# Kernel tuning notes

Hardware: AMD Instinct MI355X
Metric: run time of the kernel (lower is better)

Reference implementation:

```python
import jax, jax.numpy as jnp
import numpy as np


def setup_inputs() -> dict:
    key = jax.random.key(0)
    k1, k2 = jax.random.split(key)
    B, C, H, W = 4, 256, 64, 64
    f_m = jax.random.normal(k1, (B, C, H, W), dtype=jnp.float32)
    f_d = jax.random.normal(k2, (B, C, H, W), dtype=jnp.float32)
    return {"f_m": f_m, "f_d": f_d}


def reference(f_m, f_d):
    B, C, H, W = f_d.shape
    HW = H * W
    f_fuse = f_m + f_d                      # [B, C, H, W]
    f_c = f_fuse.reshape(B, C, HW)          # [B, C, HW]
    # scores[b, n, m] = sum_c f_c[b, c, n] * f_c[b, c, m]
    scores = jnp.einsum('bcn,bcm->bnm', f_c, f_c)   # [B, HW, HW]
    att = jax.nn.softmax(scores, axis=-1)           # softmax over last dim
    f_d_r = f_d.reshape(B, C, HW)                   # [B, C, HW]
    # out[b, c, m] = sum_n f_d_r[b, c, n] * att[b, n, m]
    f_d_att = jnp.einsum('bcn,bnm->bcm', f_d_r, att).reshape(B, C, H, W)
    return f_d_att + f_d
```

## Files before the change

### kernel.cpp

```cpp
#include <hip/hip_runtime.h>
#include <math.h>

#define B_ 4
#define C_ 256
#define N_ 4096
#define LDE 68
#define LDX 72

typedef __attribute__((ext_vector_type(8))) short short8;
typedef __attribute__((ext_vector_type(4))) float f32x4;
typedef __attribute__((ext_vector_type(2))) float f32x2;

__device__ inline ushort f2bf(float f) {
    uint u = __float_as_uint(f);
    return (ushort)((u + 0x7fffu + ((u >> 16) & 1u)) >> 16);
}
__device__ inline float bf2f(ushort h) { return __uint_as_float(((uint)h) << 16); }

__device__ inline f32x4 mfma16(short8 a, short8 b, f32x4 c) {
    return __builtin_amdgcn_mfma_f32_16x16x32_bf16(a, b, c, 0, 0, 0);
}
__device__ inline f32x4 mfma8(long a, long b, f32x4 c) {
    return __builtin_amdgcn_mfma_f32_16x16x32_fp8_fp8(a, b, c, 0, 0, 0);
}

__device__ inline size_t xfi8(int b, int nt, int kk) {
    return (((size_t)(b * 256 + nt)) * 8 + kk) * 512;
}
__device__ inline size_t ffi(int b, int nc, int ct, int k2) {
    return ((((size_t)(b * 64 + nc)) * 16 + ct) * 2 + k2) * 512;
}
__device__ inline size_t eti(int b, int mt, int ng) {
    return (((size_t)(b * 256 + mt)) * 512 + (size_t)ng) * 128;
}
__device__ inline size_t zmi(int b, int nc, int mt) {
    return ((size_t)(b * 64 + nc)) * 256 + mt;
}

__global__ __launch_bounds__(256) void prep_x_kernel(const float* __restrict__ fm,
                                                     const float* __restrict__ fd,
                                                     uchar* __restrict__ xfrag8) {
    __shared__ ushort xl[64][LDX];
    const int b = blockIdx.z, c0 = blockIdx.y * 64, n0 = blockIdx.x * 64;
    const int t = threadIdx.x;
    const int n4 = (t & 15) * 4, cl = t >> 4;
    const size_t base = (size_t)b * C_ * N_;
    #pragma unroll
    for (int p = 0; p < 4; ++p) {
        const int cr = 16 * p + cl;
        const float4 m4 = *(const float4*)(fm + base + (size_t)(c0 + cr) * N_ + n0 + n4);
        const float4 d4 = *(const float4*)(fd + base + (size_t)(c0 + cr) * N_ + n0 + n4);
        ushort4 xo;
        xo.x = f2bf(m4.x + d4.x); xo.y = f2bf(m4.y + d4.y);
        xo.z = f2bf(m4.z + d4.z); xo.w = f2bf(m4.w + d4.w);
        *(ushort4*)(&xl[cr][n4]) = xo;
    }
    __syncthreads();
    const int l = t & 63, tl = t >> 6;
    const int nl = 16 * tl + (l & 15);
    #pragma unroll
    for (int j = 0; j < 2; ++j) {
        const int kk = (c0 >> 5) + j;
        const int cb = 32 * j + 8 * (l >> 4);
        float f[8];
        #pragma unroll
        for (int i = 0; i < 8; ++i) f[i] = bf2f(xl[cb + i][nl]);
        int d0 = __builtin_amdgcn_cvt_pk_fp8_f32(f[0], f[1], 0, 0);
        d0 = __builtin_amdgcn_cvt_pk_fp8_f32(f[2], f[3], d0, 1);
        int d1 = __builtin_amdgcn_cvt_pk_fp8_f32(f[4], f[5], 0, 0);
        d1 = __builtin_amdgcn_cvt_pk_fp8_f32(f[6], f[7], d1, 1);
        uint* dst = (uint*)(xfrag8 + xfi8(b, (n0 >> 4) + tl, kk) + (size_t)l * 8);
        dst[0] = (uint)d0; dst[1] = (uint)d1;
    }
}

__global__ __launch_bounds__(512, 2) void lsum_e_kernel(const uchar* __restrict__ xfrag8,
                                                        uchar* __restrict__ E8,
                                                        uchar* __restrict__ zmask,
                                                        float* __restrict__ sinv) {
    __shared__ float red[8][64];
    const int bid = blockIdx.x;
    const int b = (bid >> 1) & 3;
    const int n0 = ((((bid >> 3) << 1) | (bid & 1))) * 64;
    const int t = threadIdx.x, lane = t & 63, w = t >> 6;
    const int l15 = lane & 15, q = lane >> 4;
    const int ph = (bid >> 3) & 31;

    long af[4][8];
    #pragma unroll
    for (int ns = 0; ns < 4; ++ns)
        #pragma unroll
        for (int kk = 0; kk < 8; ++kk)
            af[ns][kk] = *(const long*)(xfrag8 + xfi8(b, (n0 >> 4) + ns, kk) + (size_t)lane * 8);

    float dv[4][4];
    #pragma unroll
    for (int ns = 0; ns < 4; ++ns) {
        f32x4 dacc = {0.f, 0.f, 0.f, 0.f};
        #pragma unroll
        for (int kk = 0; kk < 8; ++kk)
            dacc = mfma8(af[ns][kk], af[ns][kk], dacc);
        #pragma unroll
        for (int r = 0; r < 4; ++r)
            dv[ns][r] = __shfl(dacc[r], 20 * q + r, 64);
    }

    long bn[8];
    #pragma unroll
    for (int kk = 0; kk < 8; ++kk)
        bn[kk] = *(const long*)(xfrag8 + xfi8(b, (ph & 31) * 8 + w, kk) + (size_t)lane * 8);

    const size_t ebl = (size_t)l15 * 8 + 4 * (q & 1);
    const int ngb = (n0 >> 3) + (q >> 1);
    const int ncb = n0 >> 6;

    float rs[4][4] = {};
    for (int mc = 0; mc < 32; ++mc) {
        const int cur = ((mc + ph) & 31) * 8 + w;
        const int nxt = ((mc + 1 + ph) & 31) * 8 + w;
        f32x4 a0 = {0.f,0.f,0.f,0.f}, a1 = {0.f,0.f,0.f,0.f};
        f32x4 a2 = {0.f,0.f,0.f,0.f}, a3 = {0.f,0.f,0.f,0.f};
        __builtin_amdgcn_s_setprio(1);
        #pragma unroll
        for (int kk = 0; kk < 8; ++kk) {
            const long bc = bn[kk];
            a0 = mfma8(af[0][kk], bc, a0);
            a1 = mfma8(af[1][kk], bc, a1);
            a2 = mfma8(af[2][kk], bc, a2);
            a3 = mfma8(af[3][kk], bc, a3);
            bn[kk] = *(const long*)(xfrag8 + xfi8(b, nxt, kk) + (size_t)lane * 8);
        }
        __builtin_amdgcn_s_setprio(0);
        float df[4][4];
#define EDF(AA, NS)                                                    \
        df[NS][0] = AA[0] - dv[NS][0]; df[NS][1] = AA[1] - dv[NS][1];  \
        df[NS][2] = AA[2] - dv[NS][2]; df[NS][3] = AA[3] - dv[NS][3];
        EDF(a0, 0) EDF(a1, 1) EDF(a2, 2) EDF(a3, 3)
#undef EDF
        const float mx = fmaxf(
            fmaxf(fmaxf(fmaxf(df[0][0], df[0][1]), fmaxf(df[0][2], df[0][3])),
                  fmaxf(fmaxf(df[1][0], df[1][1]), fmaxf(df[1][2], df[1][3]))),
            fmaxf(fmaxf(fmaxf(df[2][0], df[2][1]), fmaxf(df[2][2], df[2][3])),
                  fmaxf(fmaxf(df[3][0], df[3][1]), fmaxf(df[3][2], df[3][3]))));
        const bool nz = (__ballot(mx > -30.0f) != 0ULL);
        if (lane == 0) zmask[zmi(b, ncb, cur)] = nz ? 1 : 0;
        if (nz) {
            uint dpk[4];
#define EEXP(NS)                                                                       \
            {                                                                          \
                float e0 = __expf(df[NS][0]), e1 = __expf(df[NS][1]);                  \
                float e2 = __expf(df[NS][2]), e3 = __expf(df[NS][3]);                  \
                rs[NS][0] += e0; rs[NS][1] += e1; rs[NS][2] += e2; rs[NS][3] += e3;    \
                int d = __builtin_amdgcn_cvt_pk_fp8_f32(e0, e1, 0, 0);                 \
                d = __builtin_amdgcn_cvt_pk_fp8_f32(e2, e3, d, 1);                     \
                dpk[NS] = (uint)d;                                                     \
            }
            EEXP(0) EEXP(1) EEXP(2) EEXP(3)
#undef EEXP
            #pragma unroll
            for (int ns = 0; ns < 4; ++ns)
                *(uint*)(E8 + eti(b, cur, ngb + 2 * ns) + ebl) = dpk[ns];
        }
    }
    #pragma unroll
    for (int off = 1; off < 16; off <<= 1)
        #pragma unroll
        for (int ns = 0; ns < 4; ++ns)
            #pragma unroll
            for (int r = 0; r < 4; ++r)
                rs[ns][r] += __shfl_xor(rs[ns][r], off, 64);
    if (l15 == 0) {
        #pragma unroll
        for (int ns = 0; ns < 4; ++ns)
            #pragma unroll
            for (int r = 0; r < 4; ++r)
                red[w][16 * ns + 4 * q + r] = rs[ns][r];
    }
    __syncthreads();
    if (t < 64) {
        float s = 0.f;
        #pragma unroll
        for (int ww = 0; ww < 8; ++ww) s += red[ww][t];
        sinv[b * N_ + n0 + t] = 1.0f / s;
    }
}

__global__ __launch_bounds__(512, 2) void out_e_kernel(const uchar* __restrict__ E8,
                                                       const uchar* __restrict__ zmask,
                                                       const float* __restrict__ sinv,
                                                       const float* __restrict__ fd32,
                                                       float* __restrict__ outp) {
    const int bid = blockIdx.x;
    const int b = (bid >> 1) & 3;
    const int m0 = ((((bid >> 3) << 1) | (bid & 1))) * 64;
    const int t = threadIdx.x, lane = t & 63, w = t >> 6;
    const int l15 = lane & 15, q = lane >> 4;
    const size_t fb = (size_t)b * C_ * N_;
    const uchar* mrow = zmask + zmi(b, 0, m0 >> 4);

    f32x4 acc[2][4];
    #pragma unroll
    for (int ct = 0; ct < 2; ++ct)
        #pragma unroll
        for (int mt = 0; mt < 4; ++mt)
            acc[ct][mt] = (f32x4){0.f, 0.f, 0.f, 0.f};

    for (int g = 0; g < 8; ++g) {
        uint mk[8];
        #pragma unroll
        for (int i = 0; i < 8; ++i)
            mk[i] = *(const uint*)(mrow + (size_t)(8 * g + i) * 256);
        #pragma unroll
        for (int i = 0; i < 8; ++i) {
            if (mk[i] == 0) continue;
            const int nc = 8 * g + i;
            const float* sv = sinv + b * N_ + 64 * nc + 8 * q;
            float4 s0[2], s1[2];
            #pragma unroll
            for (int k2 = 0; k2 < 2; ++k2) {
                s0[k2] = *(const float4*)(sv + 32 * k2);
                s1[k2] = *(const float4*)(sv + 32 * k2 + 4);
            }
            short8 fn[2][2];
            #pragma unroll
            for (int ct = 0; ct < 2; ++ct) {
                const int c = 32 * w + 16 * ct + l15;
                const float* frow = fd32 + fb + (size_t)c * N_ + 64 * nc + 8 * q;
                #pragma unroll
                for (int k2 = 0; k2 < 2; ++k2) {
                    const float4 fa = *(const float4*)(frow + 32 * k2);
                    const float4 fb4 = *(const float4*)(frow + 32 * k2 + 4);
                    union { ushort us[8]; short8 v; } u;
                    u.us[0] = f2bf(fa.x * s0[k2].x); u.us[1] = f2bf(fa.y * s0[k2].y);
                    u.us[2] = f2bf(fa.z * s0[k2].z); u.us[3] = f2bf(fa.w * s0[k2].w);
                    u.us[4] = f2bf(fb4.x * s1[k2].x); u.us[5] = f2bf(fb4.y * s1[k2].y);
                    u.us[6] = f2bf(fb4.z * s1[k2].z); u.us[7] = f2bf(fb4.w * s1[k2].w);
                    fn[ct][k2] = u.v;
                }
            }
            #pragma unroll
            for (int k2 = 0; k2 < 2; ++k2) {
                #pragma unroll
                for (int mt = 0; mt < 4; ++mt) {
                    const long e8 = *(const long*)(E8 + eti(b, (m0 >> 4) + mt, 8 * nc + 4 * k2 + q) + (size_t)l15 * 8);
                    const uint lo = (uint)(unsigned long)e8;
                    const uint hi = (uint)((unsigned long)e8 >> 32);
                    const f32x2 f01 = __builtin_amdgcn_cvt_pk_f32_fp8((int)lo, false);
                    const f32x2 f23 = __builtin_amdgcn_cvt_pk_f32_fp8((int)lo, true);
                    const f32x2 f45 = __builtin_amdgcn_cvt_pk_f32_fp8((int)hi, false);
                    const f32x2 f67 = __builtin_amdgcn_cvt_pk_f32_fp8((int)hi, true);
                    union { uint u[4]; short8 v; } be;
                    asm("v_cvt_pk_bf16_f32 %0, %1, %2" : "=v"(be.u[0]) : "v"(f01.x), "v"(f01.y));
                    asm("v_cvt_pk_bf16_f32 %0, %1, %2" : "=v"(be.u[1]) : "v"(f23.x), "v"(f23.y));
                    asm("v_cvt_pk_bf16_f32 %0, %1, %2" : "=v"(be.u[2]) : "v"(f45.x), "v"(f45.y));
                    asm("v_cvt_pk_bf16_f32 %0, %1, %2" : "=v"(be.u[3]) : "v"(f67.x), "v"(f67.y));
                    acc[0][mt] = mfma16(fn[0][k2], be.v, acc[0][mt]);
                    acc[1][mt] = mfma16(fn[1][k2], be.v, acc[1][mt]);
                }
            }
        }
    }
    #pragma unroll
    for (int ct = 0; ct < 2; ++ct)
        #pragma unroll
        for (int mt = 0; mt < 4; ++mt)
            #pragma unroll
            for (int r = 0; r < 4; ++r) {
                const int c = 32 * w + 16 * ct + 4 * q + r;
                const int m = m0 + 16 * mt + l15;
                const size_t o = fb + (size_t)c * N_ + m;
                outp[o] = acc[ct][mt][r] + fd32[o];
            }
}

__global__ __launch_bounds__(256) void prep_kernel(const float* __restrict__ fm,
                                                   const float* __restrict__ fd,
                                                   uchar* __restrict__ xfrag8,
                                                   ushort* __restrict__ ffrag) {
    __shared__ ushort xl[64][LDX];
    __shared__ ushort fl[64][LDX];
    const int b = blockIdx.z, c0 = blockIdx.y * 64, n0 = blockIdx.x * 64;
    const int t = threadIdx.x;
    const int n4 = (t & 15) * 4, cl = t >> 4;
    const size_t base = (size_t)b * C_ * N_;
    #pragma unroll
    for (int p = 0; p < 4; ++p) {
        const int cr = 16 * p + cl;
        const float4 m4 = *(const float4*)(fm + base + (size_t)(c0 + cr) * N_ + n0 + n4);
        const float4 d4 = *(const float4*)(fd + base + (size_t)(c0 + cr) * N_ + n0 + n4);
        ushort4 fo;
        fo.x = f2bf(d4.x); fo.y = f2bf(d4.y); fo.z = f2bf(d4.z); fo.w = f2bf(d4.w);
        *(ushort4*)(&fl[cr][n4]) = fo;
        ushort4 xo;
        xo.x = f2bf(m4.x + d4.x); xo.y = f2bf(m4.y + d4.y);
        xo.z = f2bf(m4.z + d4.z); xo.w = f2bf(m4.w + d4.w);
        *(ushort4*)(&xl[cr][n4]) = xo;
    }
    __syncthreads();
    const int l = t & 63, tl = t >> 6;
    {
        const int nl = 16 * tl + (l & 15);
        #pragma unroll
        for (int j = 0; j < 2; ++j) {
            const int kk = (c0 >> 5) + j;
            const int cb = 32 * j + 8 * (l >> 4);
            float f[8];
            #pragma unroll
            for (int i = 0; i < 8; ++i) f[i] = bf2f(xl[cb + i][nl]);
            int d0 = __builtin_amdgcn_cvt_pk_fp8_f32(f[0], f[1], 0, 0);
            d0 = __builtin_amdgcn_cvt_pk_fp8_f32(f[2], f[3], d0, 1);
            int d1 = __builtin_amdgcn_cvt_pk_fp8_f32(f[4], f[5], 0, 0);
            d1 = __builtin_amdgcn_cvt_pk_fp8_f32(f[6], f[7], d1, 1);
            uint* dst = (uint*)(xfrag8 + xfi8(b, (n0 >> 4) + tl, kk) + (size_t)l * 8);
            dst[0] = (uint)d0; dst[1] = (uint)d1;
        }
    }
    {
        const int row = 16 * tl + (l & 15);
        #pragma unroll
        for (int k2 = 0; k2 < 2; ++k2) {
            const int col = 32 * k2 + 8 * (l >> 4);
            const ushort4 a0 = *(const ushort4*)(&fl[row][col]);
            const ushort4 a1 = *(const ushort4*)(&fl[row][col + 4]);
            ushort* dst = ffrag + ffi(b, n0 >> 6, (c0 >> 4) + tl, k2) + l * 8;
            *(ushort4*)(dst) = a0; *(ushort4*)(dst + 4) = a1;
        }
    }
}

__global__ __launch_bounds__(512, 2) void lsum_g_kernel(const uchar* __restrict__ xfrag8,
                                                        float* __restrict__ lg) {
    __shared__ float red[8][64];
    __shared__ float dgl[64];
    const int bid = blockIdx.x;
    const int b = (bid >> 1) & 3;
    const int n0 = ((((bid >> 3) << 1) | (bid & 1))) * 64;
    const int t = threadIdx.x, lane = t & 63, w = t >> 6;
    const int l15 = lane & 15, q = lane >> 4;

    long af[4][8];
    #pragma unroll
    for (int ns = 0; ns < 4; ++ns)
        #pragma unroll
        for (int kk = 0; kk < 8; ++kk)
            af[ns][kk] = *(const long*)(xfrag8 + xfi8(b, (n0 >> 4) + ns, kk) + (size_t)lane * 8);

    float dv[4][4];
    #pragma unroll
    for (int ns = 0; ns < 4; ++ns) {
        f32x4 dacc = {0.f, 0.f, 0.f, 0.f};
        #pragma unroll
        for (int kk = 0; kk < 8; ++kk)
            dacc = mfma8(af[ns][kk], af[ns][kk], dacc);
        #pragma unroll
        for (int r = 0; r < 4; ++r)
            dv[ns][r] = __shfl(dacc[r], 20 * q + r, 64);
    }
    if (w == 0 && l15 == 0) {
        #pragma unroll
        for (int ns = 0; ns < 4; ++ns)
            #pragma unroll
            for (int r = 0; r < 4; ++r)
                dgl[16 * ns + 4 * q + r] = dv[ns][r];
    }

    long bn[8];
    #pragma unroll
    for (int kk = 0; kk < 8; ++kk)
        bn[kk] = *(const long*)(xfrag8 + xfi8(b, w, kk) + (size_t)lane * 8);

    float rs[4][4] = {};
    for (int mc = 0; mc < 32; ++mc) {
        const int mtn = (mc + 1 < 32) ? (mc + 1) * 8 + w : w;
        f32x4 a0 = {0.f,0.f,0.f,0.f}, a1 = {0.f,0.f,0.f,0.f};
        f32x4 a2 = {0.f,0.f,0.f,0.f}, a3 = {0.f,0.f,0.f,0.f};
        #pragma unroll
        for (int kk = 0; kk < 8; ++kk) {
            const long bc = bn[kk];
            a0 = mfma8(af[0][kk], bc, a0);
            a1 = mfma8(af[1][kk], bc, a1);
            a2 = mfma8(af[2][kk], bc, a2);
            a3 = mfma8(af[3][kk], bc, a3);
            bn[kk] = *(const long*)(xfrag8 + xfi8(b, mtn, kk) + (size_t)lane * 8);
        }
        #pragma unroll
        for (int r = 0; r < 4; ++r) {
            rs[0][r] += __expf(a0[r] - dv[0][r]);
            rs[1][r] += __expf(a1[r] - dv[1][r]);
            rs[2][r] += __expf(a2[r] - dv[2][r]);
            rs[3][r] += __expf(a3[r] - dv[3][r]);
        }
    }
    #pragma unroll
    for (int off = 1; off < 16; off <<= 1)
        #pragma unroll
        for (int ns = 0; ns < 4; ++ns)
            #pragma unroll
            for (int r = 0; r < 4; ++r)
                rs[ns][r] += __shfl_xor(rs[ns][r], off, 64);
    if (l15 == 0) {
        #pragma unroll
        for (int ns = 0; ns < 4; ++ns)
            #pragma unroll
            for (int r = 0; r < 4; ++r)
                red[w][16 * ns + 4 * q + r] = rs[ns][r];
    }
    __syncthreads();
    if (t < 64) {
        float s = 0.f;
        #pragma unroll
        for (int ww = 0; ww < 8; ++ww) s += red[ww][t];
        lg[b * N_ + n0 + t] = dgl[t] + __logf(s);
    }
}

__global__ __launch_bounds__(512, 2) void out_g_kernel(const uchar* __restrict__ xfrag8,
                                                       const ushort* __restrict__ ffrag,
                                                       const float* __restrict__ gg,
                                                       const float* __restrict__ fd32,
                                                       float* __restrict__ outp) {
    __shared__ ushort ET[2][64][LDE];
    const int bid = blockIdx.x;
    const int b = (bid >> 1) & 3;
    const int m0 = ((((bid >> 3) << 1) | (bid & 1))) * 64;
    const int t = threadIdx.x, lane = t & 63, w = t >> 6;
    const int l15 = lane & 15, q = lane >> 4;
    const int a = w & 3, h = w >> 2;
    const size_t fb = (size_t)b * C_ * N_;

    long bfr[2][8];
    #pragma unroll
    for (int jt = 0; jt < 2; ++jt)
        #pragma unroll
        for (int kk = 0; kk < 8; ++kk)
            bfr[jt][kk] = *(const long*)(xfrag8 + xfi8(b, (m0 >> 4) + 2 * h + jt, kk) + (size_t)lane * 8);

    f32x4 acc[2][4];
    #pragma unroll
    for (int ct = 0; ct < 2; ++ct)
        #pragma unroll
        for (int mt = 0; mt < 4; ++mt)
            acc[ct][mt] = (f32x4){0.f, 0.f, 0.f, 0.f};

    long an[8];
    #pragma unroll
    for (int kk = 0; kk < 8; ++kk)
        an[kk] = *(const long*)(xfrag8 + xfi8(b, a, kk) + (size_t)lane * 8);
    float gn[4];
    #pragma unroll
    for (int r = 0; r < 4; ++r) gn[r] = gg[b * N_ + 16 * a + 4 * q + r];

    int p = 0;
    for (int n0c = 0; n0c < N_; n0c += 64, p ^= 1) {
        const int nc = n0c >> 6;
        short8 fn[2][2];
        #pragma unroll
        for (int ct = 0; ct < 2; ++ct)
            #pragma unroll
            for (int k2 = 0; k2 < 2; ++k2)
                fn[ct][k2] = *(const short8*)(ffrag + ffi(b, nc, 2 * w + ct, k2) + lane * 8);
        float gv[4];
        #pragma unroll
        for (int r = 0; r < 4; ++r) gv[r] = gn[r];
        const int nx = (n0c + 64 < N_) ? n0c + 64 : 0;
        #pragma unroll
        for (int r = 0; r < 4; ++r) gn[r] = gg[b * N_ + nx + 16 * a + 4 * q + r];

        f32x4 s0 = {0.f, 0.f, 0.f, 0.f}, s1 = {0.f, 0.f, 0.f, 0.f};
        #pragma unroll
        for (int kk = 0; kk < 8; ++kk) {
            s0 = mfma8(an[kk], bfr[0][kk], s0);
            s1 = mfma8(an[kk], bfr[1][kk], s1);
            an[kk] = *(const long*)(xfrag8 + xfi8(b, (nx >> 4) + a, kk) + (size_t)lane * 8);
        }
        ushort4 e0, e1;
        e0.x = f2bf(__expf(s0[0] - gv[0])); e0.y = f2bf(__expf(s0[1] - gv[1]));
        e0.z = f2bf(__expf(s0[2] - gv[2])); e0.w = f2bf(__expf(s0[3] - gv[3]));
        e1.x = f2bf(__expf(s1[0] - gv[0])); e1.y = f2bf(__expf(s1[1] - gv[1]));
        e1.z = f2bf(__expf(s1[2] - gv[2])); e1.w = f2bf(__expf(s1[3] - gv[3]));
        *(ushort4*)(&ET[p][32 * h + l15][16 * a + 4 * q])      = e0;
        *(ushort4*)(&ET[p][32 * h + 16 + l15][16 * a + 4 * q]) = e1;

        asm volatile("s_waitcnt lgkmcnt(0)\n\ts_barrier" ::: "memory");

        #pragma unroll
        for (int k2 = 0; k2 < 2; ++k2) {
            #pragma unroll
            for (int mt = 0; mt < 4; ++mt) {
                const short8 be = *(const short8*)(&ET[p][16 * mt + l15][32 * k2 + 8 * q]);
                acc[0][mt] = mfma16(fn[0][k2], be, acc[0][mt]);
                acc[1][mt] = mfma16(fn[1][k2], be, acc[1][mt]);
            }
        }
    }
    #pragma unroll
    for (int ct = 0; ct < 2; ++ct)
        #pragma unroll
        for (int mt = 0; mt < 4; ++mt)
            #pragma unroll
            for (int r = 0; r < 4; ++r) {
                const int c = 32 * w + 16 * ct + 4 * q + r;
                const int m = m0 + 16 * mt + l15;
                const size_t o = fb + (size_t)c * N_ + m;
                outp[o] = acc[ct][mt][r] + fd32[o];
            }
}

extern "C" void kernel_launch(void* const* d_in, const int* in_sizes, int n_in,
                              void* d_out, int out_size, void* d_ws, size_t ws_size,
                              hipStream_t stream) {
    const float* fm = (const float*)d_in[0];
    const float* fd = (const float*)d_in[1];
    float* outp = (float*)d_out;

    const size_t xb_elts = (size_t)B_ * N_ * C_;
    const size_t e_bytes = (size_t)B_ * N_ * N_;
    const size_t z_bytes = (size_t)B_ * 64 * 256;
    const size_t s_bytes = (size_t)B_ * N_ * 4;
    const size_t need_e  = xb_elts + e_bytes + z_bytes + s_bytes;
    const size_t need_g  = xb_elts * 3 + (size_t)B_ * N_ * 4;

    uchar* xfrag8 = (uchar*)d_ws;

    if (ws_size >= need_e) {
        uchar* E8    = xfrag8 + xb_elts;
        uchar* zmask = E8 + e_bytes;
        float* sinv  = (float*)(zmask + z_bytes);
        prep_x_kernel<<<dim3(N_ / 64, C_ / 64, B_), 256, 0, stream>>>(fm, fd, xfrag8);
        lsum_e_kernel<<<dim3(256), 512, 0, stream>>>(xfrag8, E8, zmask, sinv);
        out_e_kernel<<<dim3(256), 512, 0, stream>>>(E8, zmask, sinv, fd, outp);
    } else if (ws_size >= need_g) {
        ushort* ffrag = (ushort*)(xfrag8 + xb_elts);
        float*  lg    = (float*)(xfrag8 + xb_elts * 3);
        prep_kernel<<<dim3(N_ / 64, C_ / 64, B_), 256, 0, stream>>>(fm, fd, xfrag8, ffrag);
        lsum_g_kernel<<<dim3(256), 512, 0, stream>>>(xfrag8, lg);
        out_g_kernel<<<dim3(256), 512, 0, stream>>>(xfrag8, ffrag, lg, fd, outp);
    }
}
```

Before: 121.6 us.

## Exploit score symmetry to halve S computation in row-sum kernel

The score matrix is symmetric, so each block now computes only about half the 64x64-column tiles (a parity-based ownership of pairs) plus its diagonal tile. From each tile it derives both the row-side exp sums and the transposed column-side contributions, which are accumulated through atomics into a separate buffer. Transposed tiles flagged as nonzero in the mask are recomputed in the output kernel with an fp8 MFMA and an exp, staged through shared memory, instead of being read from the stored E matrix. This roughly halves the QK^T and exp work in the first pass. In exchange it adds global atomics, a memset, extra per-iteration diagonal-norm arithmetic, and recomputation in the output pass.

```diff
diff --git a/kernel.cpp b/kernel.cpp
--- a/kernel.cpp
+++ b/kernel.cpp
@@ -74,17 +74,36 @@
     }
 }
 
-__global__ __launch_bounds__(512, 2) void lsum_e_kernel(const uchar* __restrict__ xfrag8,
+__global__ __launch_bounds__(512, 2) void lsum_t_kernel(const uchar* __restrict__ xfrag8,
                                                         uchar* __restrict__ E8,
                                                         uchar* __restrict__ zmask,
-                                                        float* __restrict__ sinv) {
+                                                        float* __restrict__ rsbase,
+                                                        float* __restrict__ rsadd,
+                                                        float* __restrict__ dgall) {
     __shared__ float red[8][64];
+    __shared__ float dgl[64];
+    __shared__ uchar chl[34];
+    __shared__ int cnt_s;
+    __shared__ uint zst[34];
     const int bid = blockIdx.x;
     const int b = (bid >> 1) & 3;
     const int n0 = ((((bid >> 3) << 1) | (bid & 1))) * 64;
+    const int j = n0 >> 6;
     const int t = threadIdx.x, lane = t & 63, w = t >> 6;
     const int l15 = lane & 15, q = lane >> 4;
-    const int ph = (bid >> 3) & 31;
+    const int g = w >> 2, wm = w & 3;
+
+    if (t == 0) {
+        int c = 0;
+        chl[c++] = (uchar)j;
+        for (int k = 0; k < 64; ++k) {
+            if (k == j) continue;
+            const bool own = (k > j) ? (((j + k) & 1) == 0) : (((j + k) & 1) == 1);
+            if (own) chl[c++] = (uchar)k;
+        }
+        cnt_s = c;
+    }
+    if (t < 34) zst[t] = 0u;
 
     long af[4][8];
     #pragma unroll
@@ -104,22 +123,39 @@
         for (int r = 0; r < 4; ++r)
             dv[ns][r] = __shfl(dacc[r], 20 * q + r, 64);
     }
+    if (w == 0 && l15 == 0) {
+        #pragma unroll
+        for (int ns = 0; ns < 4; ++ns)
+            #pragma unroll
+            for (int r = 0; r < 4; ++r)
+                dgl[16 * ns + 4 * q + r] = dv[ns][r];
+    }
+
+    __syncthreads();
+    const int cnt = cnt_s;
 
     long bn[8];
-    #pragma unroll
-    for (int kk = 0; kk < 8; ++kk)
-        bn[kk] = *(const long*)(xfrag8 + xfi8(b, (ph & 31) * 8 + w, kk) + (size_t)lane * 8);
-
+    {
+        const int mt0 = 4 * (int)chl[g] + wm;
+        #pragma unroll
+        for (int kk = 0; kk < 8; ++kk)
+            bn[kk] = *(const long*)(xfrag8 + xfi8(b, mt0, kk) + (size_t)lane * 8);
+    }
     const size_t ebl = (size_t)l15 * 8 + 4 * (q & 1);
     const int ngb = (n0 >> 3) + (q >> 1);
-    const int ncb = n0 >> 6;
 
     float rs[4][4] = {};
-    for (int mc = 0; mc < 32; ++mc) {
-        const int cur = ((mc + ph) & 31) * 8 + w;
-        const int nxt = ((mc + 1 + ph) & 31) * 8 + w;
+    for (int it = 0; it < 17; ++it) {
+        const int idx = 2 * it + g;
+        const bool valid = idx < cnt;
+        const int kc = chl[valid ? idx : 0];
+        const int mt = 4 * kc + wm;
+        int idxn = 2 * (it + 1) + g; if (idxn >= cnt) idxn = 0;
+        const int mtn = 4 * (int)chl[idxn] + wm;
+
         f32x4 a0 = {0.f,0.f,0.f,0.f}, a1 = {0.f,0.f,0.f,0.f};
         f32x4 a2 = {0.f,0.f,0.f,0.f}, a3 = {0.f,0.f,0.f,0.f};
+        float dg0 = 0.f, dg1 = 0.f, dg2 = 0.f, dg3 = 0.f;
         __builtin_amdgcn_s_setprio(1);
         #pragma unroll
         for (int kk = 0; kk < 8; ++kk) {
@@ -128,23 +164,34 @@
             a1 = mfma8(af[1][kk], bc, a1);
             a2 = mfma8(af[2][kk], bc, a2);
             a3 = mfma8(af[3][kk], bc, a3);
-            bn[kk] = *(const long*)(xfrag8 + xfi8(b, nxt, kk) + (size_t)lane * 8);
+            bn[kk] = *(const long*)(xfrag8 + xfi8(b, mtn, kk) + (size_t)lane * 8);
+            const uint lo = (uint)(unsigned long)bc;
+            const uint hi = (uint)((unsigned long)bc >> 32);
+            const f32x2 p0 = __builtin_amdgcn_cvt_pk_f32_fp8((int)lo, false);
+            const f32x2 p1 = __builtin_amdgcn_cvt_pk_f32_fp8((int)lo, true);
+            const f32x2 p2 = __builtin_amdgcn_cvt_pk_f32_fp8((int)hi, false);
+            const f32x2 p3 = __builtin_amdgcn_cvt_pk_f32_fp8((int)hi, true);
+            dg0 = fmaf(p0.x, p0.x, dg0); dg0 = fmaf(p0.y, p0.y, dg0);
+            dg1 = fmaf(p1.x, p1.x, dg1); dg1 = fmaf(p1.y, p1.y, dg1);
+            dg2 = fmaf(p2.x, p2.x, dg2); dg2 = fmaf(p2.y, p2.y, dg2);
+            dg3 = fmaf(p3.x, p3.x, dg3); dg3 = fmaf(p3.y, p3.y, dg3);
         }
         __builtin_amdgcn_s_setprio(0);
+
         float df[4][4];
 #define EDF(AA, NS)                                                    \
         df[NS][0] = AA[0] - dv[NS][0]; df[NS][1] = AA[1] - dv[NS][1];  \
         df[NS][2] = AA[2] - dv[NS][2]; df[NS][3] = AA[3] - dv[NS][3];
         EDF(a0, 0) EDF(a1, 1) EDF(a2, 2) EDF(a3, 3)
 #undef EDF
-        const float mx = fmaxf(
+        const float mxA = fmaxf(
             fmaxf(fmaxf(fmaxf(df[0][0], df[0][1]), fmaxf(df[0][2], df[0][3])),
                   fmaxf(fmaxf(df[1][0], df[1][1]), fmaxf(df[1][2], df[1][3]))),
             fmaxf(fmaxf(fmaxf(df[2][0], df[2][1]), fmaxf(df[2][2], df[2][3])),
                   fmaxf(fmaxf(df[3][0], df[3][1]), fmaxf(df[3][2], df[3][3]))));
-        const bool nz = (__ballot(mx > -30.0f) != 0ULL);
-        if (lane == 0) zmask[zmi(b, ncb, cur)] = nz ? 1 : 0;
-        if (nz) {
+        const bool nzA = valid && (__ballot(mxA > -30.0f) != 0ULL);
+        if (valid && lane == 0) zmask[zmi(b, j, mt)] = nzA ? 1 : 0;
+        if (nzA) {
             uint dpk[4];
 #define EEXP(NS)                                                                       \
             {                                                                          \
@@ -159,7 +206,39 @@
 #undef EEXP
             #pragma unroll
             for (int ns = 0; ns < 4; ++ns)
-                *(uint*)(E8 + eti(b, cur, ngb + 2 * ns) + ebl) = dpk[ns];
+                *(uint*)(E8 + eti(b, mt, ngb + 2 * ns) + ebl) = dpk[ns];
+        }
+        if (valid && kc != j) {
+            float dgm = dg0 + dg1 + dg2 + dg3;
+            dgm += __shfl_xor(dgm, 16, 64);
+            dgm += __shfl_xor(dgm, 32, 64);
+            float dfB[4][4];
+            #pragma unroll
+            for (int ns = 0; ns < 4; ++ns) {
+                dfB[ns][0] = (ns==0?a0[0]:ns==1?a1[0]:ns==2?a2[0]:a3[0]) - dgm;
+                dfB[ns][1] = (ns==0?a0[1]:ns==1?a1[1]:ns==2?a2[1]:a3[1]) - dgm;
+                dfB[ns][2] = (ns==0?a0[2]:ns==1?a1[2]:ns==2?a2[2]:a3[2]) - dgm;
+                dfB[ns][3] = (ns==0?a0[3]:ns==1?a1[3]:ns==2?a2[3]:a3[3]) - dgm;
+            }
+            uint bits = 0;
+            #pragma unroll
+            for (int ns = 0; ns < 4; ++ns) {
+                const float m2 = fmaxf(fmaxf(dfB[ns][0], dfB[ns][1]),
+                                       fmaxf(dfB[ns][2], dfB[ns][3]));
+                if (__ballot(m2 > -30.0f) != 0ULL) bits |= (1u << ns);
+            }
+            if (bits) {
+                if (lane == 0) atomicOr(&zst[idx], bits);
+                float cs = 0.f;
+                #pragma unroll
+                for (int ns = 0; ns < 4; ++ns)
+                    #pragma unroll
+                    for (int r = 0; r < 4; ++r)
+                        cs += __expf(dfB[ns][r]);
+                cs += __shfl_xor(cs, 16, 64);
+                cs += __shfl_xor(cs, 32, 64);
+                if (q == 0) atomicAdd(rsadd + b * N_ + 16 * mt + l15, cs);
+            }
         }
     }
     #pragma unroll
@@ -181,15 +260,28 @@
         float s = 0.f;
         #pragma unroll
         for (int ww = 0; ww < 8; ++ww) s += red[ww][t];
-        sinv[b * N_ + n0 + t] = 1.0f / s;
+        rsbase[b * N_ + n0 + t] = s;
+        dgall[b * N_ + n0 + t] = dgl[t];
+    }
+    if (t >= 64 && t < 64 + 33 * 4) {
+        const int ii = (t - 64) >> 2, ns = (t - 64) & 3;
+        const int idx = ii + 1;
+        if (idx < cnt) {
+            const int kc = chl[idx];
+            zmask[zmi(b, kc, 4 * j + ns)] = (((zst[idx] >> ns) & 1u) != 0u) ? 2 : 0;
+        }
     }
 }
 
 __global__ __launch_bounds__(512, 2) void out_e_kernel(const uchar* __restrict__ E8,
                                                        const uchar* __restrict__ zmask,
-                                                       const float* __restrict__ sinv,
+                                                       const float* __restrict__ rsbase,
+                                                       const float* __restrict__ rsadd,
+                                                       const float* __restrict__ dgall,
+                                                       const uchar* __restrict__ xfrag8,
                                                        const float* __restrict__ fd32,
                                                        float* __restrict__ outp) {
+    __shared__ ushort esc[8][16][66];
     const int bid = blockIdx.x;
     const int b = (bid >> 1) & 3;
     const int m0 = ((((bid >> 3) << 1) | (bid & 1))) * 64;
@@ -205,21 +297,29 @@
         for (int mt = 0; mt < 4; ++mt)
             acc[ct][mt] = (f32x4){0.f, 0.f, 0.f, 0.f};
 
-    for (int g = 0; g < 8; ++g) {
+    for (int gg = 0; gg < 8; ++gg) {
         uint mk[8];
         #pragma unroll
         for (int i = 0; i < 8; ++i)
-            mk[i] = *(const uint*)(mrow + (size_t)(8 * g + i) * 256);
+            mk[i] = *(const uint*)(mrow + (size_t)(8 * gg + i) * 256);
         #pragma unroll
         for (int i = 0; i < 8; ++i) {
-            if (mk[i] == 0) continue;
-            const int nc = 8 * g + i;
-            const float* sv = sinv + b * N_ + 64 * nc + 8 * q;
+            const uint mki = mk[i];
+            if (mki == 0) continue;
+            const int nc = 8 * gg + i;
+            const float* rb = rsbase + b * N_ + 64 * nc + 8 * q;
+            const float* ra = rsadd + b * N_ + 64 * nc + 8 * q;
             float4 s0[2], s1[2];
             #pragma unroll
             for (int k2 = 0; k2 < 2; ++k2) {
-                s0[k2] = *(const float4*)(sv + 32 * k2);
-                s1[k2] = *(const float4*)(sv + 32 * k2 + 4);
+                const float4 b0 = *(const float4*)(rb + 32 * k2);
+                const float4 b1 = *(const float4*)(rb + 32 * k2 + 4);
+                const float4 a0v = *(const float4*)(ra + 32 * k2);
+                const float4 a1v = *(const float4*)(ra + 32 * k2 + 4);
+                s0[k2].x = 1.0f / (b0.x + a0v.x); s0[k2].y = 1.0f / (b0.y + a0v.y);
+                s0[k2].z = 1.0f / (b0.z + a0v.z); s0[k2].w = 1.0f / (b0.w + a0v.w);
+                s1[k2].x = 1.0f / (b1.x + a1v.x); s1[k2].y = 1.0f / (b1.y + a1v.y);
+                s1[k2].z = 1.0f / (b1.z + a1v.z); s1[k2].w = 1.0f / (b1.w + a1v.w);
             }
             short8 fn[2][2];
             #pragma unroll
@@ -238,24 +338,57 @@
                     fn[ct][k2] = u.v;
                 }
             }
-            #pragma unroll
-            for (int k2 = 0; k2 < 2; ++k2) {
+            if ((mki & ~0x01010101u) == 0u) {
+                #pragma unroll
+                for (int k2 = 0; k2 < 2; ++k2) {
+                    #pragma unroll
+                    for (int mt = 0; mt < 4; ++mt) {
+                        if (((mki >> (8 * mt)) & 0xffu) != 1u) continue;
+                        const long e8 = *(const long*)(E8 + eti(b, (m0 >> 4) + mt, 8 * nc + 4 * k2 + q) + (size_t)l15 * 8);
+                        const uint lo = (uint)(unsigned long)e8;
+                        const uint hi = (uint)((unsigned long)e8 >> 32);
+                        const f32x2 f01 = __builtin_amdgcn_cvt_pk_f32_fp8((int)lo, false);
+                        const f32x2 f23 = __builtin_amdgcn_cvt_pk_f32_fp8((int)lo, true);
+                        const f32x2 f45 = __builtin_amdgcn_cvt_pk_f32_fp8((int)hi, false);
+                        const f32x2 f67 = __builtin_amdgcn_cvt_pk_f32_fp8((int)hi, true);
+                        union { uint u[4]; short8 v; } be;
+                        asm("v_cvt_pk_bf16_f32 %0, %1, %2" : "=v"(be.u[0]) : "v"(f01.x), "v"(f01.y));
+                        asm("v_cvt_pk_bf16_f32 %0, %1, %2" : "=v"(be.u[1]) : "v"(f23.x), "v"(f23.y));
+                        asm("v_cvt_pk_bf16_f32 %0, %1, %2" : "=v"(be.u[2]) : "v"(f45.x), "v"(f45.y));
+                        asm("v_cvt_pk_bf16_f32 %0, %1, %2" : "=v"(be.u[3]) : "v"(f67.x), "v"(f67.y));
+                        acc[0][mt] = mfma16(fn[0][k2], be.v, acc[0][mt]);
+                        acc[1][mt] = mfma16(fn[1][k2], be.v, acc[1][mt]);
+                    }
+                }
+            } else {
                 #pragma unroll
                 for (int mt = 0; mt < 4; ++mt) {
-                    const long e8 = *(const long*)(E8 + eti(b, (m0 >> 4) + mt, 8 * nc + 4 * k2 + q) + (size_t)l15 * 8);
-                    const uint lo = (uint)(unsigned long)e8;
-                    const uint hi = (uint)((unsigned long)e8 >> 32);
-                    const f32x2 f01 = __builtin_amdgcn_cvt_pk_f32_fp8((int)lo, false);
-                    const f32x2 f23 = __builtin_amdgcn_cvt_pk_f32_fp8((int)lo, true);
-                    const f32x2 f45 = __builtin_amdgcn_cvt_pk_f32_fp8((int)hi, false);
-                    const f32x2 f67 = __builtin_amdgcn_cvt_pk_f32_fp8((int)hi, true);
-                    union { uint u[4]; short8 v; } be;
-                    asm("v_cvt_pk_bf16_f32 %0, %1, %2" : "=v"(be.u[0]) : "v"(f01.x), "v"(f01.y));
-                    asm("v_cvt_pk_bf16_f32 %0, %1, %2" : "=v"(be.u[1]) : "v"(f23.x), "v"(f23.y));
-                    asm("v_cvt_pk_bf16_f32 %0, %1, %2" : "=v"(be.u[2]) : "v"(f45.x), "v"(f45.y));
-                    asm("v_cvt_pk_bf16_f32 %0, %1, %2" : "=v"(be.u[3]) : "v"(f67.x), "v"(f67.y));
-                    acc[0][mt] = mfma16(fn[0][k2], be.v, acc[0][mt]);
-                    acc[1][mt] = mfma16(fn[1][k2], be.v, acc[1][mt]);
+                    long bmf[8];
+                    #pragma unroll
+                    for (int kk = 0; kk < 8; ++kk)
+                        bmf[kk] = *(const long*)(xfrag8 + xfi8(b, (m0 >> 4) + mt, kk) + (size_t)lane * 8);
+                    #pragma unroll
+                    for (int nt = 0; nt < 4; ++nt) {
+                        long anf[8];
+                        #pragma unroll
+                        for (int kk = 0; kk < 8; ++kk)
+                            anf[kk] = *(const long*)(xfrag8 + xfi8(b, 4 * nc + nt, kk) + (size_t)lane * 8);
+                        f32x4 sacc = {0.f, 0.f, 0.f, 0.f};
+                        #pragma unroll
+                        for (int kk = 0; kk < 8; ++kk)
+                            sacc = mfma8(anf[kk], bmf[kk], sacc);
+                        #pragma unroll
+                        for (int r = 0; r < 4; ++r) {
+                            const float gv = dgall[b * N_ + 64 * nc + 16 * nt + 4 * q + r];
+                            esc[w][l15][16 * nt + 4 * q + r] = f2bf(__expf(sacc[r] - gv));
+                        }
+                    }
+                    #pragma unroll
+                    for (int k2 = 0; k2 < 2; ++k2) {
+                        const short8 be = *(const short8*)(&esc[w][l15][32 * k2 + 8 * q]);
+                        acc[0][mt] = mfma16(fn[0][k2], be, acc[0][mt]);
+                        acc[1][mt] = mfma16(fn[1][k2], be, acc[1][mt]);
+                    }
                 }
             }
         }
@@ -516,19 +649,22 @@
     const size_t xb_elts = (size_t)B_ * N_ * C_;
     const size_t e_bytes = (size_t)B_ * N_ * N_;
     const size_t z_bytes = (size_t)B_ * 64 * 256;
-    const size_t s_bytes = (size_t)B_ * N_ * 4;
-    const size_t need_e  = xb_elts + e_bytes + z_bytes + s_bytes;
-    const size_t need_g  = xb_elts * 3 + (size_t)B_ * N_ * 4;
+    const size_t f_bytes = (size_t)B_ * N_ * 4;
+    const size_t need_e  = xb_elts + e_bytes + z_bytes + 3 * f_bytes;
+    const size_t need_g  = xb_elts * 3 + f_bytes;
 
     uchar* xfrag8 = (uchar*)d_ws;
 
     if (ws_size >= need_e) {
-        uchar* E8    = xfrag8 + xb_elts;
-        uchar* zmask = E8 + e_bytes;
-        float* sinv  = (float*)(zmask + z_bytes);
+        uchar* E8     = xfrag8 + xb_elts;
+        uchar* zmask  = E8 + e_bytes;
+        float* rsbase = (float*)(zmask + z_bytes);
+        float* rsadd  = rsbase + (size_t)B_ * N_;
+        float* dgall  = rsadd + (size_t)B_ * N_;
+        hipMemsetAsync(rsadd, 0, f_bytes, stream);
         prep_x_kernel<<<dim3(N_ / 64, C_ / 64, B_), 256, 0, stream>>>(fm, fd, xfrag8);
-        lsum_e_kernel<<<dim3(256), 512, 0, stream>>>(xfrag8, E8, zmask, sinv);
-        out_e_kernel<<<dim3(256), 512, 0, stream>>>(E8, zmask, sinv, fd, outp);
+        lsum_t_kernel<<<dim3(256), 512, 0, stream>>>(xfrag8, E8, zmask, rsbase, rsadd, dgall);
+        out_e_kernel<<<dim3(256), 512, 0, stream>>>(E8, zmask, rsbase, rsadd, dgall, xfrag8, fd, outp);
     } else if (ws_size >= need_g) {
         ushort* ffrag = (ushort*)(xfrag8 + xb_elts);
         float*  lg    = (float*)(xfrag8 + xb_elts * 3);
```

After: 115.1 us. 1.06x faster.
